# Optimization experiments

Hardware: AMD Instinct MI355X
Metric: run time of the kernel (lower is better)

## Reference

```python
import jax, jax.numpy as jnp
import numpy as np

NEG_BIG = -9.0e15  # mask value used by the torch module
LEAKY_SLOPE = 0.01  # torch nn.LeakyReLU default


def setup_inputs() -> dict:
    key = jax.random.key(0)
    k1, k2, k3, k4 = jax.random.split(key, 4)
    N, F_in, F_out = 8192, 256, 128
    x = jax.random.normal(k1, (N, F_in), dtype=jnp.float32)
    adj = jax.random.randint(k2, (N, N), 0, 2, dtype=jnp.int32)
    W = jax.random.normal(k3, (F_in, F_out), dtype=jnp.float32) * 0.05
    a = jax.random.normal(k4, (2 * F_out, 1), dtype=jnp.float32) * 0.05
    return {"x": x, "adj": adj, "W": W, "a": a}


def reference(x, adj, W, a):
    F_out = W.shape[1]
    h = x @ W                                   # [N, F_out]
    # e[i, j] = leaky_relu([h_i || h_j] . a) = leaky_relu(h_i.a1 + h_j.a2)
    a1, a2 = a[:F_out, 0], a[F_out:, 0]
    e = h @ a1[:, None] + (h @ a2)[None, :]     # [N, N]
    e = jax.nn.leaky_relu(e, negative_slope=LEAKY_SLOPE)
    scores = jnp.where(adj > 0, e, NEG_BIG)
    attention = jax.nn.softmax(scores, axis=1)  # dropout p=0 -> identity
    h1 = jax.nn.elu(attention @ h)              # [N, F_out]
    return h1, attention
```

## Files before the change

kernel.cpp:

```cpp
#include <hip/hip_runtime.h>

#define N 8192
#define FI 256
#define FO 128

typedef short bf16x8 __attribute__((ext_vector_type(8)));
typedef float f32x4 __attribute__((ext_vector_type(4)));
typedef unsigned short u16x4 __attribute__((ext_vector_type(4)));
typedef unsigned long long u64;
typedef u64 u64x2 __attribute__((ext_vector_type(2)));

static __device__ __forceinline__ unsigned short f2bf(float x) {
  unsigned int u = __builtin_bit_cast(unsigned int, x);
  u = (u + 0x7fffu + ((u >> 16) & 1u)) >> 16;
  return (unsigned short)u;
}
static __device__ __forceinline__ float lrelu(float x) {
  return fmaxf(x, 0.01f * x);
}

__global__ __launch_bounds__(256) void k_prep(
    const float* __restrict__ x, const float* __restrict__ W, const float* __restrict__ a,
    unsigned short* __restrict__ h_t, float* __restrict__ ha1, float* __restrict__ ha2) {
  __shared__ float xs[16][256];
  __shared__ float redA[16][2], redB[16][2];
  const int t = threadIdx.x;
  const int i0 = blockIdx.x * 16;
  #pragma unroll
  for (int ii = 0; ii < 16; ++ii)
    xs[ii][t & 255] = x[(long long)(i0 + ii) * FI + t];
  __syncthreads();
  const int rg = t >> 7;
  const int f = t & 127;
  float accs[8] = {0.f, 0.f, 0.f, 0.f, 0.f, 0.f, 0.f, 0.f};
  for (int k = 0; k < 256; ++k) {
    const float wv = W[k * FO + f];
    #pragma unroll
    for (int rr = 0; rr < 8; ++rr) accs[rr] = fmaf(xs[rg * 8 + rr][k], wv, accs[rr]);
  }
  {
    ushort4 s0, s1;
    s0.x = f2bf(accs[0]); s0.y = f2bf(accs[1]); s0.z = f2bf(accs[2]); s0.w = f2bf(accs[3]);
    s1.x = f2bf(accs[4]); s1.y = f2bf(accs[5]); s1.z = f2bf(accs[6]); s1.w = f2bf(accs[7]);
    unsigned short* dst = h_t + (long long)f * N + i0 + rg * 8;
    *(ushort4*)dst = s0;
    *(ushort4*)(dst + 4) = s1;
  }
  const float a1f = a[f];
  const float a2f = a[FO + f];
  const int lane = t & 63;
  const int wig = (t >> 6) & 1;
  #pragma unroll
  for (int rr = 0; rr < 8; ++rr) {
    float v1 = accs[rr] * a1f;
    float v2 = accs[rr] * a2f;
    #pragma unroll
    for (int off = 32; off; off >>= 1) { v1 += __shfl_xor(v1, off); v2 += __shfl_xor(v2, off); }
    if (lane == 0) { redA[rg * 8 + rr][wig] = v1; redB[rg * 8 + rr][wig] = v2; }
  }
  __syncthreads();
  if (t < 16) {
    ha1[i0 + t] = redA[t][0] + redA[t][1];
    ha2[i0 + t] = redB[t][0] + redB[t][1];
  }
}

template <int WM>
__global__ __launch_bounds__(256) void k_mask(
    const int* __restrict__ adj, const float* __restrict__ ha1g, const float* __restrict__ ha2g,
    u64* __restrict__ msk, float* __restrict__ lse_row) {
  const int t = threadIdx.x;
  const int lane = t & 63;
  const int row = blockIdx.x * 4 + (t >> 6);
  const float ei = ha1g[row];
  const int* __restrict__ arow = adj + (size_t)row * N;
  u64* __restrict__ mrow = msk + (size_t)row * 128;
  float m = -3.0e38f, s = 0.f;
  for (int it = 0; it < 32; ++it) {
    const int j0 = it * 256 + lane * 4;
    const int4 a4 = *(const int4*)(arow + j0);
    const float4 h2 = *(const float4*)(ha2g + j0);
    const bool b0 = a4.x > 0, b1 = a4.y > 0, b2 = a4.z > 0, b3 = a4.w > 0;
    #define ONLINE(bb, vv) { \
      const float t0 = ei + (vv); \
      const float e = lrelu(t0); \
      const float mn = (bb) ? fmaxf(m, e) : m; \
      s = fmaf(s, __expf(m - mn), (bb) ? __expf(e - mn) : 0.f); \
      m = mn; }
    ONLINE(b0, h2.x) ONLINE(b1, h2.y) ONLINE(b2, h2.z) ONLINE(b3, h2.w)
    #undef ONLINE
    if (WM) {
      const u64 q0 = __ballot(b0), q1 = __ballot(b1);
      const u64 q2 = __ballot(b2), q3 = __ballot(b3);
      if (lane == 0) {
        u64x2 v01 = {q0, q1}, v23 = {q2, q3};
        *(u64x2*)(mrow + it * 4) = v01;
        *(u64x2*)(mrow + it * 4 + 2) = v23;
      }
    }
  }
  #pragma unroll
  for (int off = 32; off; off >>= 1) {
    const float mo = __shfl_xor(m, off);
    const float so = __shfl_xor(s, off);
    const float mn = fmaxf(m, mo);
    s = s * __expf(m - mn) + so * __expf(mo - mn);
    m = mn;
  }
  if (lane == 0) lse_row[row] = (s > 0.f) ? (m + __logf(s)) : 3.0e38f;
}

template <int UA>
__global__ __launch_bounds__(512) void k_pv(
    const int* __restrict__ adj, const u64* __restrict__ msk,
    const unsigned short* __restrict__ h_t, const float* __restrict__ ha1g,
    const float* __restrict__ ha2g, const float* __restrict__ lse_row,
    float* __restrict__ h1, float* __restrict__ attn) {
  __shared__ unsigned short p_lds[2][16][136];
  const int t = threadIdx.x;
  const int lane = t & 63;
  const int w = t >> 6;
  const int base = blockIdx.x * 16;
  const int pr = t >> 5;
  const int pjw = t & 31;
  const float ei = ha1g[base + pr];
  const float nls = lse_row[base + pr];
  const u64* __restrict__ mrow = msk + (size_t)(base + pr) * 128;
  const int* __restrict__ arow = adj + (size_t)(base + pr) * N;
  float* __restrict__ atrow = attn + (size_t)(base + pr) * N;

  const int f0 = w * 16;
  const unsigned short* __restrict__ hbase =
      h_t + (size_t)(f0 + (lane & 15)) * N + (lane >> 4) * 8;
  const unsigned short* pfrag0 = &p_lds[0][lane & 15][(lane >> 4) * 8];

  f32x4 acc = {0.f, 0.f, 0.f, 0.f};

  auto compute_p = [&](int jt) {
    const int j = jt * 128 + pjw * 4;
    bool b0, b1, b2, b3;
    if constexpr (UA) {
      const int4 a4 = *(const int4*)(arow + j);
      b0 = a4.x > 0; b1 = a4.y > 0; b2 = a4.z > 0; b3 = a4.w > 0;
    } else {
      const int it = j >> 8;
      const int l = (j >> 2) & 63;
      const u64x2 qa = *(const u64x2*)(mrow + it * 4);
      const u64x2 qb = *(const u64x2*)(mrow + it * 4 + 2);
      b0 = (qa.x >> l) & 1; b1 = (qa.y >> l) & 1;
      b2 = (qb.x >> l) & 1; b3 = (qb.y >> l) & 1;
    }
    const float4 h2 = *(const float4*)(ha2g + j);
    const float p0 = b0 ? __expf(lrelu(ei + h2.x) - nls) : 0.f;
    const float p1 = b1 ? __expf(lrelu(ei + h2.y) - nls) : 0.f;
    const float p2 = b2 ? __expf(lrelu(ei + h2.z) - nls) : 0.f;
    const float p3 = b3 ? __expf(lrelu(ei + h2.w) - nls) : 0.f;
    f32x4 pv = {p0, p1, p2, p3};
    __builtin_nontemporal_store(pv, (f32x4*)(atrow + j));
    u16x4 pb = {f2bf(p0), f2bf(p1), f2bf(p2), f2bf(p3)};
    *(u16x4*)&p_lds[(jt & 1)][pr][pjw * 4] = pb;
  };

  bf16x8 hA[4], hB[4];
  compute_p(0);
  #pragma unroll
  for (int ks = 0; ks < 4; ++ks) hA[ks] = *(const bf16x8*)(hbase + ks * 32);
  __syncthreads();

  for (int jt = 0; jt < 64; ++jt) {
    if (jt < 63) {
      compute_p(jt + 1);
      #pragma unroll
      for (int ks = 0; ks < 4; ++ks)
        hB[ks] = *(const bf16x8*)(hbase + (jt + 1) * 128 + ks * 32);
    }
    const unsigned short* pf = pfrag0 + (jt & 1) * (16 * 136);
    #pragma unroll
    for (int ks = 0; ks < 4; ++ks) {
      const bf16x8 av = *(const bf16x8*)(pf + ks * 32);
      acc = __builtin_amdgcn_mfma_f32_16x16x32_bf16(av, hA[ks], acc, 0, 0, 0);
    }
    if (jt < 63) {
      __syncthreads();
      #pragma unroll
      for (int ks = 0; ks < 4; ++ks) hA[ks] = hB[ks];
    }
  }
  {
    const int rbase = (lane >> 4) * 4;
    const int col = lane & 15;
    #pragma unroll
    for (int rgi = 0; rgi < 4; ++rgi) {
      float v = acc[rgi];
      v = v > 0.f ? v : __expf(v) - 1.f;
      h1[(long long)(base + rbase + rgi) * FO + f0 + col] = v;
    }
  }
}

extern "C" void kernel_launch(void* const* d_in, const int* in_sizes, int n_in,
                              void* d_out, int out_size, void* d_ws, size_t ws_size,
                              hipStream_t stream) {
  const float* x = (const float*)d_in[0];
  const int* adj = (const int*)d_in[1];
  const float* W = (const float*)d_in[2];
  const float* a = (const float*)d_in[3];
  float* h1 = (float*)d_out;
  float* attn = (float*)d_out + (size_t)N * FO;

  char* wsb = (char*)d_ws;
  unsigned short* h_t = (unsigned short*)wsb;
  float* ha1 = (float*)(wsb + (size_t)FO * N * 2);
  float* ha2 = ha1 + N;
  float* lse = ha2 + N;
  const size_t msk_off = (size_t)FO * N * 2 + 3 * (size_t)N * 4;
  u64* msk = (u64*)(wsb + msk_off);
  const size_t need = msk_off + (size_t)N * 128 * 8;

  k_prep<<<N / 16, 256, 0, stream>>>(x, W, a, h_t, ha1, ha2);
  if (ws_size >= need) {
    k_mask<1><<<N / 4, 256, 0, stream>>>(adj, ha1, ha2, msk, lse);
    k_pv<0><<<N / 16, 512, 0, stream>>>(adj, msk, h_t, ha1, ha2, lse, h1, attn);
  } else {
    k_mask<0><<<N / 4, 256, 0, stream>>>(adj, ha1, ha2, msk, lse);
    k_pv<1><<<N / 16, 512, 0, stream>>>(adj, msk, h_t, ha1, ha2, lse, h1, attn);
  }
}
```

Measured before the change: 237.1 us.

## Replace online softmax with max-then-sum, stage ha2 in LDS, relax barriers

The mask kernel now caches the whole ha2 vector in shared memory and replaces the per-element online softmax (two exps per element) with a two-pass scheme. It first takes the row max of the masked ha2, using the fact that leaky ReLU is monotonic, then sums exponentials using mask bits kept in registers. In the PV kernel, __syncthreads is replaced by a barrier that waits only on LDS counters, so outstanding global loads and stores are not drained at each step. The costs are 32KB of LDS per block in k_mask, which may reduce occupancy, and a second loop over LDS.

```diff
diff --git a/kernel.cpp b/kernel.cpp
--- a/kernel.cpp
+++ b/kernel.cpp
@@ -17,6 +17,11 @@
 }
 static __device__ __forceinline__ float lrelu(float x) {
   return fmaxf(x, 0.01f * x);
+}
+static __device__ __forceinline__ void barrier_lds() {
+  asm volatile("s_waitcnt lgkmcnt(0)" ::: "memory");
+  __builtin_amdgcn_s_barrier();
+  asm volatile("" ::: "memory");
 }
 
 __global__ __launch_bounds__(256) void k_prep(
@@ -69,26 +74,34 @@
 __global__ __launch_bounds__(256) void k_mask(
     const int* __restrict__ adj, const float* __restrict__ ha1g, const float* __restrict__ ha2g,
     u64* __restrict__ msk, float* __restrict__ lse_row) {
+  __shared__ float h2s[N];
   const int t = threadIdx.x;
   const int lane = t & 63;
+  #pragma unroll
+  for (int i = 0; i < 8; ++i) {
+    const int idx = i * 1024 + t * 4;
+    *(float4*)&h2s[idx] = *(const float4*)(ha2g + idx);
+  }
+  __syncthreads();
   const int row = blockIdx.x * 4 + (t >> 6);
   const float ei = ha1g[row];
   const int* __restrict__ arow = adj + (size_t)row * N;
   u64* __restrict__ mrow = msk + (size_t)row * 128;
-  float m = -3.0e38f, s = 0.f;
+  unsigned int bits0 = 0, bits1 = 0, bits2 = 0, bits3 = 0;
+  float mloc = -3.0e38f;
   for (int it = 0; it < 32; ++it) {
     const int j0 = it * 256 + lane * 4;
     const int4 a4 = *(const int4*)(arow + j0);
-    const float4 h2 = *(const float4*)(ha2g + j0);
+    const float4 h2 = *(const float4*)&h2s[j0];
     const bool b0 = a4.x > 0, b1 = a4.y > 0, b2 = a4.z > 0, b3 = a4.w > 0;
-    #define ONLINE(bb, vv) { \
-      const float t0 = ei + (vv); \
-      const float e = lrelu(t0); \
-      const float mn = (bb) ? fmaxf(m, e) : m; \
-      s = fmaf(s, __expf(m - mn), (bb) ? __expf(e - mn) : 0.f); \
-      m = mn; }
-    ONLINE(b0, h2.x) ONLINE(b1, h2.y) ONLINE(b2, h2.z) ONLINE(b3, h2.w)
-    #undef ONLINE
+    bits0 |= (b0 ? 1u : 0u) << it;
+    bits1 |= (b1 ? 1u : 0u) << it;
+    bits2 |= (b2 ? 1u : 0u) << it;
+    bits3 |= (b3 ? 1u : 0u) << it;
+    mloc = fmaxf(mloc, b0 ? h2.x : -3.0e38f);
+    mloc = fmaxf(mloc, b1 ? h2.y : -3.0e38f);
+    mloc = fmaxf(mloc, b2 ? h2.z : -3.0e38f);
+    mloc = fmaxf(mloc, b3 ? h2.w : -3.0e38f);
     if (WM) {
       const u64 q0 = __ballot(b0), q1 = __ballot(b1);
       const u64 q2 = __ballot(b2), q3 = __ballot(b3);
@@ -100,13 +113,20 @@
     }
   }
   #pragma unroll
-  for (int off = 32; off; off >>= 1) {
-    const float mo = __shfl_xor(m, off);
-    const float so = __shfl_xor(s, off);
-    const float mn = fmaxf(m, mo);
-    s = s * __expf(m - mn) + so * __expf(mo - mn);
-    m = mn;
-  }
+  for (int off = 32; off; off >>= 1) mloc = fmaxf(mloc, __shfl_xor(mloc, off));
+  const float m = lrelu(ei + mloc);
+  float s0 = 0.f, s1 = 0.f, s2 = 0.f, s3 = 0.f;
+  for (int it = 0; it < 32; ++it) {
+    const int j0 = it * 256 + lane * 4;
+    const float4 h2 = *(const float4*)&h2s[j0];
+    s0 += ((bits0 >> it) & 1) ? __expf(lrelu(ei + h2.x) - m) : 0.f;
+    s1 += ((bits1 >> it) & 1) ? __expf(lrelu(ei + h2.y) - m) : 0.f;
+    s2 += ((bits2 >> it) & 1) ? __expf(lrelu(ei + h2.z) - m) : 0.f;
+    s3 += ((bits3 >> it) & 1) ? __expf(lrelu(ei + h2.w) - m) : 0.f;
+  }
+  float s = (s0 + s1) + (s2 + s3);
+  #pragma unroll
+  for (int off = 32; off; off >>= 1) s += __shfl_xor(s, off);
   if (lane == 0) lse_row[row] = (s > 0.f) ? (m + __logf(s)) : 3.0e38f;
 }
 
@@ -165,7 +185,7 @@
   compute_p(0);
   #pragma unroll
   for (int ks = 0; ks < 4; ++ks) hA[ks] = *(const bf16x8*)(hbase + ks * 32);
-  __syncthreads();
+  barrier_lds();
 
   for (int jt = 0; jt < 64; ++jt) {
     if (jt < 63) {
@@ -181,7 +201,7 @@
       acc = __builtin_amdgcn_mfma_f32_16x16x32_bf16(av, hA[ks], acc, 0, 0, 0);
     }
     if (jt < 63) {
-      __syncthreads();
+      barrier_lds();
       #pragma unroll
       for (int ks = 0; ks < 4; ++ks) hA[ks] = hB[ks];
     }
```

Measured after the change: 271.0 us. +14.3%, slower.

## Split PV reduction across waves by key range and drop LDS P exchange

Applied to the files above, without the earlier changes.

Restructures the attention-times-h kernel so each wave owns a disjoint 1024-column slice of the keys for all 16 rows and all 128 features. Each wave builds its own bf16 P fragment directly in registers, so the shared P buffer and the per-step block barrier go away. Partial results are reduced with LDS atomics at the end. This trades the barrier and LDS traffic for more accumulator registers, strided h_t gathers without prefetch, regular rather than nontemporal attention stores, and an atomic reduction.

```diff
diff --git a/kernel.cpp b/kernel.cpp
--- a/kernel.cpp
+++ b/kernel.cpp
@@ -6,7 +6,6 @@
 
 typedef short bf16x8 __attribute__((ext_vector_type(8)));
 typedef float f32x4 __attribute__((ext_vector_type(4)));
-typedef unsigned short u16x4 __attribute__((ext_vector_type(4)));
 typedef unsigned long long u64;
 typedef u64 u64x2 __attribute__((ext_vector_type(2)));
 
@@ -116,85 +115,90 @@
     const unsigned short* __restrict__ h_t, const float* __restrict__ ha1g,
     const float* __restrict__ ha2g, const float* __restrict__ lse_row,
     float* __restrict__ h1, float* __restrict__ attn) {
-  __shared__ unsigned short p_lds[2][16][136];
+  __shared__ float red[16][128];
   const int t = threadIdx.x;
   const int lane = t & 63;
   const int w = t >> 6;
   const int base = blockIdx.x * 16;
-  const int pr = t >> 5;
-  const int pjw = t & 31;
-  const float ei = ha1g[base + pr];
-  const float nls = lse_row[base + pr];
-  const u64* __restrict__ mrow = msk + (size_t)(base + pr) * 128;
-  const int* __restrict__ arow = adj + (size_t)(base + pr) * N;
-  float* __restrict__ atrow = attn + (size_t)(base + pr) * N;
-
-  const int f0 = w * 16;
-  const unsigned short* __restrict__ hbase =
-      h_t + (size_t)(f0 + (lane & 15)) * N + (lane >> 4) * 8;
-  const unsigned short* pfrag0 = &p_lds[0][lane & 15][(lane >> 4) * 8];
-
-  f32x4 acc = {0.f, 0.f, 0.f, 0.f};
-
-  auto compute_p = [&](int jt) {
-    const int j = jt * 128 + pjw * 4;
-    bool b0, b1, b2, b3;
+  const int r = lane & 15;
+  const int jc = lane >> 4;
+  const int row = base + r;
+  const float ei = ha1g[row];
+  const float nls = lse_row[row];
+  const u64* __restrict__ mrow = msk + (size_t)row * 128;
+  const int* __restrict__ arow = adj + (size_t)row * N;
+  float* __restrict__ atrow = attn + (size_t)row * N;
+  const int jbase = w * 1024;
+
+  f32x4 acc[8];
+  #pragma unroll
+  for (int f = 0; f < 8; ++f) acc[f] = (f32x4){0.f, 0.f, 0.f, 0.f};
+
+  for (int jt = 0; jt < 32; ++jt) {
+    const int j0 = jbase + jt * 32 + jc * 8;
+    unsigned int bits8;
     if constexpr (UA) {
-      const int4 a4 = *(const int4*)(arow + j);
-      b0 = a4.x > 0; b1 = a4.y > 0; b2 = a4.z > 0; b3 = a4.w > 0;
+      const int4 a0 = *(const int4*)(arow + j0);
+      const int4 a1 = *(const int4*)(arow + j0 + 4);
+      bits8 = (a0.x > 0 ? 1u : 0u) | (a0.y > 0 ? 2u : 0u) | (a0.z > 0 ? 4u : 0u) |
+              (a0.w > 0 ? 8u : 0u) | (a1.x > 0 ? 16u : 0u) | (a1.y > 0 ? 32u : 0u) |
+              (a1.z > 0 ? 64u : 0u) | (a1.w > 0 ? 128u : 0u);
     } else {
-      const int it = j >> 8;
-      const int l = (j >> 2) & 63;
+      const int it = j0 >> 8;
+      const int l = (j0 >> 2) & 63;
       const u64x2 qa = *(const u64x2*)(mrow + it * 4);
       const u64x2 qb = *(const u64x2*)(mrow + it * 4 + 2);
-      b0 = (qa.x >> l) & 1; b1 = (qa.y >> l) & 1;
-      b2 = (qb.x >> l) & 1; b3 = (qb.y >> l) & 1;
+      const unsigned int n0 = (unsigned int)((qa.x >> l) & 3ull);
+      const unsigned int n1 = (unsigned int)((qa.y >> l) & 3ull);
+      const unsigned int n2 = (unsigned int)((qb.x >> l) & 3ull);
+      const unsigned int n3 = (unsigned int)((qb.y >> l) & 3ull);
+      bits8 = (n0 & 1u) | ((n1 & 1u) << 1) | ((n2 & 1u) << 2) | ((n3 & 1u) << 3) |
+              ((n0 >> 1) << 4) | ((n1 >> 1) << 5) | ((n2 >> 1) << 6) | ((n3 >> 1) << 7);
     }
-    const float4 h2 = *(const float4*)(ha2g + j);
-    const float p0 = b0 ? __expf(lrelu(ei + h2.x) - nls) : 0.f;
-    const float p1 = b1 ? __expf(lrelu(ei + h2.y) - nls) : 0.f;
-    const float p2 = b2 ? __expf(lrelu(ei + h2.z) - nls) : 0.f;
-    const float p3 = b3 ? __expf(lrelu(ei + h2.w) - nls) : 0.f;
-    f32x4 pv = {p0, p1, p2, p3};
-    __builtin_nontemporal_store(pv, (f32x4*)(atrow + j));
-    u16x4 pb = {f2bf(p0), f2bf(p1), f2bf(p2), f2bf(p3)};
-    *(u16x4*)&p_lds[(jt & 1)][pr][pjw * 4] = pb;
-  };
-
-  bf16x8 hA[4], hB[4];
-  compute_p(0);
-  #pragma unroll
-  for (int ks = 0; ks < 4; ++ks) hA[ks] = *(const bf16x8*)(hbase + ks * 32);
-  __syncthreads();
-
-  for (int jt = 0; jt < 64; ++jt) {
-    if (jt < 63) {
-      compute_p(jt + 1);
-      #pragma unroll
-      for (int ks = 0; ks < 4; ++ks)
-        hB[ks] = *(const bf16x8*)(hbase + (jt + 1) * 128 + ks * 32);
+    const float4 hA = *(const float4*)(ha2g + j0);
+    const float4 hB = *(const float4*)(ha2g + j0 + 4);
+    float p[8];
+    p[0] = (bits8 & 1u)   ? __expf(lrelu(ei + hA.x) - nls) : 0.f;
+    p[1] = (bits8 & 2u)   ? __expf(lrelu(ei + hA.y) - nls) : 0.f;
+    p[2] = (bits8 & 4u)   ? __expf(lrelu(ei + hA.z) - nls) : 0.f;
+    p[3] = (bits8 & 8u)   ? __expf(lrelu(ei + hA.w) - nls) : 0.f;
+    p[4] = (bits8 & 16u)  ? __expf(lrelu(ei + hB.x) - nls) : 0.f;
+    p[5] = (bits8 & 32u)  ? __expf(lrelu(ei + hB.y) - nls) : 0.f;
+    p[6] = (bits8 & 64u)  ? __expf(lrelu(ei + hB.z) - nls) : 0.f;
+    p[7] = (bits8 & 128u) ? __expf(lrelu(ei + hB.w) - nls) : 0.f;
+    *(float4*)(atrow + j0) = make_float4(p[0], p[1], p[2], p[3]);
+    *(float4*)(atrow + j0 + 4) = make_float4(p[4], p[5], p[6], p[7]);
+    union { bf16x8 v; unsigned short us[8]; } avu;
+    avu.us[0] = f2bf(p[0]); avu.us[1] = f2bf(p[1]);
+    avu.us[2] = f2bf(p[2]); avu.us[3] = f2bf(p[3]);
+    avu.us[4] = f2bf(p[4]); avu.us[5] = f2bf(p[5]);
+    avu.us[6] = f2bf(p[6]); avu.us[7] = f2bf(p[7]);
+    const bf16x8 av = avu.v;
+    #pragma unroll
+    for (int f = 0; f < 8; ++f) {
+      const bf16x8 bv = *(const bf16x8*)(h_t + (size_t)(f * 16 + r) * N + j0);
+      acc[f] = __builtin_amdgcn_mfma_f32_16x16x32_bf16(av, bv, acc[f], 0, 0, 0);
     }
-    const unsigned short* pf = pfrag0 + (jt & 1) * (16 * 136);
-    #pragma unroll
-    for (int ks = 0; ks < 4; ++ks) {
-      const bf16x8 av = *(const bf16x8*)(pf + ks * 32);
-      acc = __builtin_amdgcn_mfma_f32_16x16x32_bf16(av, hA[ks], acc, 0, 0, 0);
-    }
-    if (jt < 63) {
-      __syncthreads();
-      #pragma unroll
-      for (int ks = 0; ks < 4; ++ks) hA[ks] = hB[ks];
-    }
-  }
+  }
+
+  *(float4*)&red[t >> 5][(t & 31) * 4] = make_float4(0.f, 0.f, 0.f, 0.f);
+  __syncthreads();
+  #pragma unroll
+  for (int f = 0; f < 8; ++f) {
+    #pragma unroll
+    for (int i = 0; i < 4; ++i)
+      atomicAdd(&red[jc * 4 + i][f * 16 + r], acc[f][i]);
+  }
+  __syncthreads();
   {
-    const int rbase = (lane >> 4) * 4;
-    const int col = lane & 15;
-    #pragma unroll
-    for (int rgi = 0; rgi < 4; ++rgi) {
-      float v = acc[rgi];
-      v = v > 0.f ? v : __expf(v) - 1.f;
-      h1[(long long)(base + rbase + rgi) * FO + f0 + col] = v;
-    }
+    const int orow = t >> 5;
+    const int oc = (t & 31) * 4;
+    float4 v = *(float4*)&red[orow][oc];
+    v.x = v.x > 0.f ? v.x : __expf(v.x) - 1.f;
+    v.y = v.y > 0.f ? v.y : __expf(v.y) - 1.f;
+    v.z = v.z > 0.f ? v.z : __expf(v.z) - 1.f;
+    v.w = v.w > 0.f ? v.w : __expf(v.w) - 1.f;
+    *(float4*)(h1 + (size_t)(base + orow) * FO + oc) = v;
   }
 }
 
```

Result: slower. 337.9 us (+42.6%).
